# Kernel optimization log

Measured on AMD Instinct MI355X. Metric: run time of the kernel, lower is better.

The kernel has to match this reference:

```python
import jax, jax.numpy as jnp
import numpy as np
import math

EPS = 1e-6
C = 0.01

def _norm(x):
    return jnp.maximum(jnp.linalg.norm(x, axis=-1, keepdims=True), EPS)

def project_to_ball(x, c=C):
    max_norm = 1.0 / math.sqrt(c) - EPS
    norm = _norm(x)
    clamped = jnp.minimum(norm, max_norm - EPS)
    return x * (clamped / norm)

def log_map_zero(x, c=C):
    sqrt_c = math.sqrt(c)
    xn = _norm(x)
    scaled = jnp.minimum(sqrt_c * xn, 1.0 - EPS)
    return jnp.arctanh(scaled) * x / (sqrt_c * xn)

def exp_map_zero(v, c=C):
    sqrt_c = math.sqrt(c)
    vn = _norm(v)
    res = jnp.tanh(sqrt_c * vn) * (v / vn) / sqrt_c
    return project_to_ball(res, c)

def setup_inputs() -> dict:
    key = jax.random.key(0)
    k1, k2, k3 = jax.random.split(key, 3)
    N, d_in, d_out = 262144, 256, 256
    x = jax.random.normal(k1, (N, d_in), dtype=jnp.float32)
    # xavier_uniform with relu gain = sqrt(2)
    gain = math.sqrt(2.0)
    bound = gain * math.sqrt(6.0 / (d_in + d_out))
    W = jax.random.uniform(k2, (d_out, d_in), dtype=jnp.float32, minval=-bound, maxval=bound)
    b = jnp.zeros((d_out,), dtype=jnp.float32)
    return {"x": x, "W": W, "b": b}

def reference(x, W, b):
    tangent = log_map_zero(x)                      # [N, d_in]
    transformed = tangent @ W.T + b                # [N, d_out]
    return exp_map_zero(transformed)               # [N, d_out]
```

## Files before the change

kernel.cpp:

```cpp
#include <hip/hip_runtime.h>
#include <stdint.h>

typedef float f32x4 __attribute__((ext_vector_type(4)));
typedef __bf16 bf16x8 __attribute__((ext_vector_type(8)));

__device__ __forceinline__ unsigned int pack_bf16_rne(float fa, float fb) {
  unsigned int ua = __float_as_uint(fa);
  ua += 0x7fffu + ((ua >> 16) & 1u);
  unsigned int ub = __float_as_uint(fb);
  ub += 0x7fffu + ((ub >> 16) & 1u);
  return __builtin_amdgcn_perm(ub, ua, 0x07060302u);
}

__global__ void wcvt_kernel(const float* __restrict__ W, uint2* __restrict__ Wb) {
  int i = blockIdx.x * blockDim.x + threadIdx.x;
  float4 v = ((const float4*)W)[i];
  uint2 o;
  o.x = pack_bf16_rne(v.x, v.y);
  o.y = pack_bf16_rne(v.z, v.w);
  Wb[i] = o;
}

__device__ __forceinline__ void convert_tile(float4 g0, float4 g1, float4 g2,
                                             float4 g3, int lane, int w,
                                             unsigned char* As, float* a_scale) {
  float p0 = g0.x * g0.x + g0.y * g0.y + g0.z * g0.z + g0.w * g0.w;
  float p1 = g1.x * g1.x + g1.y * g1.y + g1.z * g1.z + g1.w * g1.w;
  float p2 = g2.x * g2.x + g2.y * g2.y + g2.z * g2.z + g2.w * g2.w;
  float p3 = g3.x * g3.x + g3.y * g3.y + g3.z * g3.z + g3.w * g3.w;
#pragma unroll
  for (int m = 1; m < 64; m <<= 1) {
    p0 += __shfl_xor(p0, m);
    p1 += __shfl_xor(p1, m);
    p2 += __shfl_xor(p2, m);
    p3 += __shfl_xor(p3, m);
  }
  float pv = p0;
  pv = (lane == 1) ? p1 : pv;
  pv = (lane == 2) ? p2 : pv;
  pv = (lane == 3) ? p3 : pv;
  if (lane < 4) {
    float xn = fmaxf(sqrtf(pv), 1e-6f);
    float t = fminf(0.1f * xn, 1.0f - 1e-6f);
    a_scale[w + 8 * lane] = atanhf(t) / (0.1f * xn);
  }
  const int physoff = (((lane >> 1) ^ w) << 4) + (lane & 1) * 8;
#pragma unroll
  for (int i = 0; i < 4; ++i) {
    float4 gg = (i == 0) ? g0 : (i == 1) ? g1 : (i == 2) ? g2 : g3;
    uint2 o;
    o.x = pack_bf16_rne(gg.x, gg.y);
    o.y = pack_bf16_rne(gg.z, gg.w);
    *(uint2*)(As + (w + 8 * i) * 512 + physoff) = o;
  }
}

__global__ __launch_bounds__(512, 4) void hyper_kernel(
    const float* __restrict__ x, const unsigned short* __restrict__ Wb,
    const float* __restrict__ bias, float* __restrict__ out, int nt) {
  __shared__ __align__(16) unsigned char As[32 * 512];
  __shared__ float a_scale[32];
  __shared__ float rowsq[32][8];
  __shared__ float oscale[32];

  const int tid = threadIdx.x;
  const int w = tid >> 6;
  const int lane = tid & 63;
  const int l15 = lane & 15;
  const int l4 = lane >> 4;
  const int swz = l15 & 7;

  int tile = blockIdx.x;
  if (tile >= nt) return;

  bf16x8 breg[2][8];
#pragma unroll
  for (int tc = 0; tc < 2; ++tc) {
    const unsigned short* wp = Wb + (w * 32 + tc * 16 + l15) * 256 + l4 * 8;
#pragma unroll
    for (int s = 0; s < 8; ++s) breg[tc][s] = *(const bf16x8*)(wp + s * 32);
  }
  float bv[2];
#pragma unroll
  for (int tc = 0; tc < 2; ++tc) bv[tc] = bias[w * 32 + tc * 16 + l15];

  {
    const float4* xp = (const float4*)x + (size_t)tile * 2048 + tid;
    float4 g0 = xp[0], g1 = xp[512], g2 = xp[1024], g3 = xp[1536];
    convert_tile(g0, g1, g2, g3, lane, w, As, a_scale);
  }
  __syncthreads();

  for (;;) {
    const int next = tile + (int)gridDim.x;
    const bool hn = next < nt;
    float4 g0, g1, g2, g3;
    if (hn) {
      const float4* xp = (const float4*)x + (size_t)next * 2048 + tid;
      g0 = xp[0];
      g1 = xp[512];
      g2 = xp[1024];
      g3 = xp[1536];
    }
    __builtin_amdgcn_sched_barrier(0);

    const f32x4 fzero = {0.f, 0.f, 0.f, 0.f};
    f32x4 acc[2][2];
#pragma unroll
    for (int a = 0; a < 2; ++a)
#pragma unroll
      for (int b = 0; b < 2; ++b) acc[a][b] = fzero;

#pragma unroll
    for (int s = 0; s < 8; ++s) {
      bf16x8 af[2];
#pragma unroll
      for (int tr = 0; tr < 2; ++tr) {
        int ar = tr * 16 + l15;
        af[tr] = *(const bf16x8*)(As + ar * 512 + (((s * 4 + l4) ^ swz) << 4));
      }
#pragma unroll
      for (int tr = 0; tr < 2; ++tr)
#pragma unroll
        for (int tc = 0; tc < 2; ++tc)
          acc[tr][tc] = __builtin_amdgcn_mfma_f32_16x16x32_bf16(
              af[tr], breg[tc][s], acc[tr][tc], 0, 0, 0);
    }

#pragma unroll
    for (int tr = 0; tr < 2; ++tr)
#pragma unroll
      for (int rg = 0; rg < 4; ++rg) {
        int lr = tr * 16 + l4 * 4 + rg;
        float as = a_scale[lr];
        float v0 = acc[tr][0][rg] * as + bv[0];
        float v1 = acc[tr][1][rg] * as + bv[1];
        acc[tr][0][rg] = v0;
        acc[tr][1][rg] = v1;
        float s = v0 * v0 + v1 * v1;
        s += __shfl_xor(s, 1);
        s += __shfl_xor(s, 2);
        s += __shfl_xor(s, 4);
        s += __shfl_xor(s, 8);
        if (l15 == 0) rowsq[lr][w] = s;
      }
    __syncthreads();

    if (tid < 32) {
      float ssq = rowsq[tid][0] + rowsq[tid][1] + rowsq[tid][2] + rowsq[tid][3] +
                  rowsq[tid][4] + rowsq[tid][5] + rowsq[tid][6] + rowsq[tid][7];
      float norm = sqrtf(ssq);
      float vn = fmaxf(norm, 1e-6f);
      float a1 = tanhf(0.1f * vn) / (0.1f * vn);
      float rn = fmaxf(norm * a1, 1e-6f);
      float cl = fminf(rn, 10.0f - 2e-6f);
      oscale[tid] = a1 * (cl / rn);
    }
    if (hn) convert_tile(g0, g1, g2, g3, lane, w, As, a_scale);
    __syncthreads();

    float* op = out + (size_t)tile * 8192 + w * 32 + l15;
#pragma unroll
    for (int tr = 0; tr < 2; ++tr)
#pragma unroll
      for (int rg = 0; rg < 4; ++rg) {
        int lr = tr * 16 + l4 * 4 + rg;
        float os = oscale[lr];
#pragma unroll
        for (int tc = 0; tc < 2; ++tc)
          op[lr * 256 + tc * 16] = acc[tr][tc][rg] * os;
      }

    if (!hn) break;
    tile = next;
  }
}

extern "C" void kernel_launch(void* const* d_in, const int* in_sizes, int n_in,
                              void* d_out, int out_size, void* d_ws, size_t ws_size,
                              hipStream_t stream) {
  const float* x = (const float*)d_in[0];
  const float* W = (const float*)d_in[1];
  const float* bias = (const float*)d_in[2];
  float* out = (float*)d_out;
  const int N = in_sizes[0] / 256;
  const int wgrid = in_sizes[1] / 1024;
  const int nt = N / 32;

  wcvt_kernel<<<wgrid, 256, 0, stream>>>(W, (uint2*)d_ws);
  const int grid = nt < 512 ? nt : 512;
  hyper_kernel<<<grid, 512, 0, stream>>>(x, (const unsigned short*)d_ws, bias,
                                         out, nt);
}
```

Measured before the change: 472.0 us.

## Double-buffer A tile and drop a barrier by computing row scales per thread

Double-buffers the shared A tile, its row scales and the row-sum buffers. This lets the next tile be converted into the other buffer without waiting, so one __syncthreads per iteration is removed. The output-scale computation (tanh, sqrt) is now done redundantly by every thread rather than by 32 threads writing to a shared array. Launch bounds raise the occupancy hint from 4 to 6 blocks and the grid grows from 512 to 768, which increases register pressure and shared-memory use per block.

```diff
diff --git a/kernel.cpp b/kernel.cpp
--- a/kernel.cpp
+++ b/kernel.cpp
@@ -55,13 +55,12 @@
   }
 }
 
-__global__ __launch_bounds__(512, 4) void hyper_kernel(
+__global__ __launch_bounds__(512, 6) void hyper_kernel(
     const float* __restrict__ x, const unsigned short* __restrict__ Wb,
     const float* __restrict__ bias, float* __restrict__ out, int nt) {
-  __shared__ __align__(16) unsigned char As[32 * 512];
-  __shared__ float a_scale[32];
-  __shared__ float rowsq[32][8];
-  __shared__ float oscale[32];
+  __shared__ __align__(16) unsigned char As[2][32 * 512];
+  __shared__ float a_scale[2][32];
+  __shared__ __align__(16) float rowsq[2][32][8];
 
   const int tid = threadIdx.x;
   const int w = tid >> 6;
@@ -87,10 +86,11 @@
   {
     const float4* xp = (const float4*)x + (size_t)tile * 2048 + tid;
     float4 g0 = xp[0], g1 = xp[512], g2 = xp[1024], g3 = xp[1536];
-    convert_tile(g0, g1, g2, g3, lane, w, As, a_scale);
+    convert_tile(g0, g1, g2, g3, lane, w, As[0], a_scale[0]);
   }
   __syncthreads();
 
+  int buf = 0;
   for (;;) {
     const int next = tile + (int)gridDim.x;
     const bool hn = next < nt;
@@ -104,6 +104,7 @@
     }
     __builtin_amdgcn_sched_barrier(0);
 
+    const unsigned char* Ab = As[buf];
     const f32x4 fzero = {0.f, 0.f, 0.f, 0.f};
     f32x4 acc[2][2];
 #pragma unroll
@@ -117,7 +118,7 @@
 #pragma unroll
       for (int tr = 0; tr < 2; ++tr) {
         int ar = tr * 16 + l15;
-        af[tr] = *(const bf16x8*)(As + ar * 512 + (((s * 4 + l4) ^ swz) << 4));
+        af[tr] = *(const bf16x8*)(Ab + ar * 512 + (((s * 4 + l4) ^ swz) << 4));
       }
 #pragma unroll
       for (int tr = 0; tr < 2; ++tr)
@@ -132,7 +133,7 @@
 #pragma unroll
       for (int rg = 0; rg < 4; ++rg) {
         int lr = tr * 16 + l4 * 4 + rg;
-        float as = a_scale[lr];
+        float as = a_scale[buf][lr];
         float v0 = acc[tr][0][rg] * as + bv[0];
         float v1 = acc[tr][1][rg] * as + bv[1];
         acc[tr][0][rg] = v0;
@@ -142,21 +143,10 @@
         s += __shfl_xor(s, 2);
         s += __shfl_xor(s, 4);
         s += __shfl_xor(s, 8);
-        if (l15 == 0) rowsq[lr][w] = s;
+        if (l15 == 0) rowsq[buf][lr][w] = s;
       }
-    __syncthreads();
 
-    if (tid < 32) {
-      float ssq = rowsq[tid][0] + rowsq[tid][1] + rowsq[tid][2] + rowsq[tid][3] +
-                  rowsq[tid][4] + rowsq[tid][5] + rowsq[tid][6] + rowsq[tid][7];
-      float norm = sqrtf(ssq);
-      float vn = fmaxf(norm, 1e-6f);
-      float a1 = tanhf(0.1f * vn) / (0.1f * vn);
-      float rn = fmaxf(norm * a1, 1e-6f);
-      float cl = fminf(rn, 10.0f - 2e-6f);
-      oscale[tid] = a1 * (cl / rn);
-    }
-    if (hn) convert_tile(g0, g1, g2, g3, lane, w, As, a_scale);
+    if (hn) convert_tile(g0, g1, g2, g3, lane, w, As[buf ^ 1], a_scale[buf ^ 1]);
     __syncthreads();
 
     float* op = out + (size_t)tile * 8192 + w * 32 + l15;
@@ -165,14 +155,22 @@
 #pragma unroll
       for (int rg = 0; rg < 4; ++rg) {
         int lr = tr * 16 + l4 * 4 + rg;
-        float os = oscale[lr];
-#pragma unroll
-        for (int tc = 0; tc < 2; ++tc)
-          op[lr * 256 + tc * 16] = acc[tr][tc][rg] * os;
+        const float4* rp = (const float4*)rowsq[buf][lr];
+        float4 r0 = rp[0], r1 = rp[1];
+        float ssq = r0.x + r0.y + r0.z + r0.w + r1.x + r1.y + r1.z + r1.w;
+        float norm = sqrtf(ssq);
+        float vn = fmaxf(norm, 1e-6f);
+        float a1 = tanhf(0.1f * vn) / (0.1f * vn);
+        float rn = fmaxf(norm * a1, 1e-6f);
+        float cl = fminf(rn, 10.0f - 2e-6f);
+        float os = a1 * (cl / rn);
+        op[lr * 256] = acc[tr][0][rg] * os;
+        op[lr * 256 + 16] = acc[tr][1][rg] * os;
       }
 
     if (!hn) break;
     tile = next;
+    buf ^= 1;
   }
 }
 
@@ -188,7 +186,7 @@
   const int nt = N / 32;
 
   wcvt_kernel<<<wgrid, 256, 0, stream>>>(W, (uint2*)d_ws);
-  const int grid = nt < 512 ? nt : 512;
+  const int grid = nt < 768 ? nt : 768;
   hyper_kernel<<<grid, 512, 0, stream>>>(x, (const unsigned short*)d_ws, bias,
                                          out, nt);
 }
```

New measurement: 592.4 us. +25.5%, slower.
